# Kernel optimization log

Hardware: AMD Instinct MI355X
Metric: run time of the kernel (lower is better)

The kernel has to match this reference:

```python
import jax, jax.numpy as jnp
import numpy as np

DIM = 256; CTX_DIM = 256; K = 7; SK = 5; NH = 4  # num_heads*2
HD = DIM // NH; SCALE = HD ** -0.5
H = 64; W = 64; HC = 56; WC = 56
LN_EPS = 1e-6; BN_EPS = 1e-5


def make_bias_idx(k, h, w):
    # Faithful port of ContMix.generate_idx + apply_rpb index construction.
    rs = 2 * k - 1
    idx_h = np.arange(k); idx_w = np.arange(k)
    idx_k = (idx_h[:, None] * rs + idx_w).reshape(-1)
    rep_h = np.ones(k, np.int64); rep_h[k // 2] = h - (k - 1)
    rep_w = np.ones(k, np.int64); rep_w[k // 2] = w - (k - 1)
    bias_hw = np.repeat(idx_h, rep_h)[:, None] * rs + np.repeat(idx_w, rep_w)  # (h, w)
    bias_idx = (bias_hw[..., None] + idx_k).reshape(-1, k * k)                 # (h*w, k^2)
    return jnp.asarray(bias_idx[::-1].copy())  # torch.flip along dim 0


def window_idx(n, k):
    # NATTEN-style clamped neighborhood window starts.
    s = np.clip(np.arange(n) - k // 2, 0, n - k)
    return jnp.asarray(s[:, None] + np.arange(k))  # (n, k)


BIDX1 = make_bias_idx(SK, H, W)
BIDX2 = make_bias_idx(K, H, W)
IDXI_S = window_idx(H, SK); IDXJ_S = window_idx(W, SK)
IDXI_L = window_idx(H, K);  IDXJ_L = window_idx(W, K)


def ln2d(x, g, b):
    # LayerNorm over channel dim per spatial location, x: (B, C, H, W)
    mu = x.mean(1, keepdims=True)
    var = ((x - mu) ** 2).mean(1, keepdims=True)
    return (x - mu) * jax.lax.rsqrt(var + LN_EPS) * g[None, :, None, None] + b[None, :, None, None]


def conv1x1(x, Wt):
    return jnp.einsum('oc,bchw->bohw', Wt, x)


def apply_rpb(attn, rpb, bias_idx, h, w):
    g = rpb.shape[0]
    r = rpb.reshape(g, -1)[:, bias_idx]  # (g, h*w, k^2)
    return attn + r.reshape(1, g, h, w, -1)


def na2d_av(attn, value, k, idx_i, idx_j):
    # attn: (B, G, H, W, k^2), value: (B, G, H, W, C)
    B, G, h, w, _ = attn.shape
    v = value[:, :, idx_i]        # (B, G, H, k, W, C)
    v = v[:, :, :, :, idx_j]      # (B, G, H, k, W, k, C)
    a = attn.reshape(B, G, h, w, k, k)
    return jnp.einsum('bghwpq,bghpwqc->bghwc', a, v)


def contmix_forward(x, ctx, Wq, gq, bq, Wk, gk, bk, Wproj, rpb1, rpb2, Wdy, bn_g, bn_b):
    B = x.shape[0]
    q = ln2d(conv1x1(x, Wq), gq, bq) * SCALE                       # (B, DIM, H, W)
    # AdaptiveAvgPool2d(7) on 56x56 -> exact 8x8 bins
    kctx = ctx.reshape(B, CTX_DIM, 7, HC // 7, 7, WC // 7).mean((3, 5))
    kf = ln2d(conv1x1(kctx, Wk), gk, bk)                            # (B, DIM, 7, 7)
    q = q.reshape(B, NH, HD, H * W)
    kf = kf.reshape(B, NH, HD, 49)
    wgt = jnp.einsum('bgcn,bgcl->bgnl', q, kf)                      # (B, 4, HW, 49)
    wgt = jnp.einsum('ml,bgnl->bgnm', Wproj, wgt)                   # (B, 4, HW, 74)
    wgt = wgt.reshape(B, NH, H, W, SK * SK + K * K)
    attn1 = wgt[:, :NH // 2, :, :, :SK * SK]                        # group1, 25
    attn2 = wgt[:, NH // 2:, :, :, SK * SK:]                        # group2, 49
    attn1 = jax.nn.softmax(apply_rpb(attn1, rpb1, BIDX1, H, W), -1)
    attn2 = jax.nn.softmax(apply_rpb(attn2, rpb2, BIDX2, H, W), -1)
    # 'b (m g c) h w -> m b g h w c', m=2, g=2
    v = x.reshape(B, 2, NH // 2, HD, H, W).transpose(1, 0, 2, 4, 5, 3)
    x1 = na2d_av(attn1, v[0], SK, IDXI_S, IDXJ_S)                   # (B, 2, H, W, HD)
    x2 = na2d_av(attn2, v[1], K, IDXI_L, IDXJ_L)
    out = jnp.concatenate([x1, x2], axis=1)                         # (B, 4, H, W, HD)
    out = out.transpose(0, 1, 4, 2, 3).reshape(B, DIM, H, W)
    out = conv1x1(out, Wdy)
    # BatchNorm2d in eval mode: running_mean=0, running_var=1
    out = out * (bn_g * jax.lax.rsqrt(jnp.float32(1.0) + BN_EPS))[None, :, None, None] + bn_b[None, :, None, None]
    return out


def setup_inputs() -> dict:
    key = jax.random.key(0)
    ks = jax.random.split(key, 10)
    d = {}
    d['x'] = jax.random.normal(ks[0], (4, DIM, H, W), jnp.float32)
    d['ctx'] = jax.random.normal(ks[1], (4, CTX_DIM, HC, WC), jnp.float32)
    d['Wq'] = jax.random.normal(ks[2], (DIM, DIM), jnp.float32) * 0.02
    d['gq'] = jnp.ones((DIM,), jnp.float32)
    d['bq'] = jnp.zeros((DIM,), jnp.float32)
    d['Wk'] = jax.random.normal(ks[3], (DIM, CTX_DIM), jnp.float32) * 0.02
    d['gk'] = jnp.ones((DIM,), jnp.float32)
    d['bk'] = jnp.zeros((DIM,), jnp.float32)
    d['Wproj'] = jax.random.normal(ks[4], (SK * SK + K * K, 49), jnp.float32) * 0.1
    d['rpb1'] = jax.random.normal(ks[5], (NH // 2, 2 * SK - 1, 2 * SK - 1), jnp.float32) * 0.02
    d['rpb2'] = jax.random.normal(ks[6], (NH // 2, 2 * K - 1, 2 * K - 1), jnp.float32) * 0.02
    d['Wdy'] = jax.random.normal(ks[7], (DIM, DIM), jnp.float32) * 0.02
    d['bn_g'] = jnp.ones((DIM,), jnp.float32)
    d['bn_b'] = jnp.zeros((DIM,), jnp.float32)
    return d


def reference(x, ctx, Wq, gq, bq, Wk, gk, bk, Wproj, rpb1, rpb2, Wdy, bn_g, bn_b):
    return contmix_forward(x, ctx, Wq, gq, bq, Wk, gk, bk, Wproj, rpb1, rpb2, Wdy, bn_g, bn_b)
```

## Files before the change

### kernel.cpp

```cpp
#include <hip/hip_runtime.h>

#define DEV __device__ __forceinline__

typedef __bf16 bf16x8 __attribute__((ext_vector_type(8)));
typedef __bf16 bf16x4 __attribute__((ext_vector_type(4)));
typedef float floatx4 __attribute__((ext_vector_type(4)));

__global__ __launch_bounds__(256)
void prep_kernel(const float* __restrict__ Wq, const float* __restrict__ Wdy,
                 const float* __restrict__ ctx, const float* __restrict__ x,
                 __bf16* __restrict__ wqb, __bf16* __restrict__ wdyb,
                 float* __restrict__ kctx, __bf16* __restrict__ xt) {
  __shared__ float tile[64][65];
  int bid = blockIdx.x, t = threadIdx.x;
  if (bid < 256) {
    int i = bid * 256 + t;
    wqb[i]  = (__bf16)Wq[i];
    wdyb[i] = (__bf16)Wdy[i];
  } else if (bid < 512) {
    int bc = (bid - 256) * 4 + (t >> 6);
    const float* src = ctx + (size_t)bc * (56 * 56);
    int w = t & 63;
#pragma unroll
    for (int pi = 0; pi < 7; ++pi) {
      float s = 0.f;
      if (w < 56) {
#pragma unroll
        for (int di = 0; di < 8; ++di) s += src[(pi * 8 + di) * 56 + w];
      }
      s += __shfl_down(s, 4);
      s += __shfl_down(s, 2);
      s += __shfl_down(s, 1);
      if (w < 56 && (w & 7) == 0)
        kctx[(size_t)bc * 49 + pi * 7 + (w >> 3)] = s * (1.f / 64.f);
    }
  } else {
    int idx = bid - 512;
    int b = idx >> 8, c0 = ((idx >> 6) & 3) * 64, n0 = (idx & 63) * 64;
    int lane = t & 63, rg = t >> 6;
    const float* src = x + ((size_t)b * 256 + c0) * 4096 + n0;
    for (int i = rg; i < 64; i += 4) tile[i][lane] = src[(size_t)i * 4096 + lane];
    __syncthreads();
    __bf16* dst = xt + ((size_t)b * 4096 + n0) * 256 + c0;
    for (int i = rg; i < 64; i += 4) dst[(size_t)i * 256 + lane] = (__bf16)tile[lane][i];
  }
}

__global__ __launch_bounds__(256)
void kf_ln_kernel(const float* __restrict__ kctx, const float* __restrict__ Wk,
                  const float* __restrict__ gk, const float* __restrict__ bk,
                  float* __restrict__ kf) {
  int b = blockIdx.x / 49, l = blockIdx.x % 49;
  __shared__ float xs[256];
  __shared__ float r1[4], r2[4];
  int o = threadIdx.x;
  xs[o] = kctx[((size_t)b * 256 + o) * 49 + l];
  __syncthreads();
  const float* wrow = Wk + (size_t)o * 256;
  float acc = 0.f;
#pragma unroll 8
  for (int c = 0; c < 256; c += 4) {
    float4 wv = *(const float4*)(wrow + c);
    acc += wv.x * xs[c] + wv.y * xs[c + 1] + wv.z * xs[c + 2] + wv.w * xs[c + 3];
  }
  float s1 = acc, s2 = acc * acc;
#pragma unroll
  for (int off = 32; off > 0; off >>= 1) {
    s1 += __shfl_down(s1, off);
    s2 += __shfl_down(s2, off);
  }
  int wv_ = o >> 6, ln = o & 63;
  if (ln == 0) { r1[wv_] = s1; r2[wv_] = s2; }
  __syncthreads();
  float mu  = (r1[0] + r1[1] + r1[2] + r1[3]) * (1.f / 256.f);
  float var = (r2[0] + r2[1] + r2[2] + r2[3]) * (1.f / 256.f) - mu * mu;
  float rstd = rsqrtf(var + 1e-6f);
  kf[((size_t)b * 256 + o) * 49 + l] = (acc - mu) * rstd * gk[o] + bk[o];
}

__global__ __launch_bounds__(256)
void kfp_kernel(const float* __restrict__ kf, const float* __restrict__ Wproj,
                __bf16* __restrict__ kfpT) {
  int bg = blockIdx.x; int b = bg >> 2, g = bg & 3;
  int m0 = blockIdx.y * 16;
  __shared__ float kfs[64][50];
  __shared__ float wps[16][50];
  int t = threadIdx.x;
  for (int i = t; i < 64 * 49; i += 256) {
    int d = i / 49, l = i % 49;
    kfs[d][l] = kf[((size_t)b * 256 + g * 64 + d) * 49 + l];
  }
  for (int i = t; i < 16 * 49; i += 256) {
    int m = i / 49, l = i % 49;
    wps[m][l] = (m0 + m < 74) ? Wproj[(m0 + m) * 49 + l] : 0.f;
  }
  __syncthreads();
  for (int i = t; i < 64 * 16; i += 256) {
    int d = i >> 4, m = i & 15;
    float s = 0.f;
    if (m0 + m < 74) {
#pragma unroll 7
      for (int l = 0; l < 49; ++l) s += kfs[d][l] * wps[m][l];
    }
    kfpT[(size_t)bg * 5120 + (m0 + m) * 64 + d] = (__bf16)s;
  }
}

DEV int rep_idx(int p, int kc, int t1, int sub) {
  return p < kc ? p : (p < t1 ? kc : p - sub);
}

template <int KK>
DEV void softmax_write(const float* wms, const float* rpb_s, __bf16* __restrict__ attnL,
                       int bg, int n_glob, int row) {
  constexpr int CNT = KK * KK;
  constexpr int RS  = 2 * KK - 1;
  constexpr int KC  = KK / 2;
  constexpr int T1  = KC + (64 - KK + 1);
  constexpr int SUB = 64 - KK;
  constexpr int MLO = (KK == 5) ? 0 : 25;
  constexpr int PW  = (KK == 5) ? 32 : 56;
  int h = n_glob >> 6, w = n_glob & 63;
  int rh = rep_idx(63 - h, KC, T1, SUB);
  int rw = rep_idx(63 - w, KC, T1, SUB);
  float vals[CNT];
  float mx = -1e30f;
#pragma unroll
  for (int m = 0; m < CNT; ++m) {
    int ki = m / KK, kj = m % KK;
    float v = wms[row * 81 + MLO + m] + rpb_s[(rh + ki) * RS + rw + kj];
    vals[m] = v; mx = fmaxf(mx, v);
  }
  float ssum = 0.f;
#pragma unroll
  for (int m = 0; m < CNT; ++m) { float e = __expf(vals[m] - mx); vals[m] = e; ssum += e; }
  float inv = 1.f / ssum;
  __bf16 hv[PW];
#pragma unroll
  for (int m = 0; m < PW; ++m) hv[m] = (__bf16)(m < CNT ? vals[m] * inv : 0.f);
  __bf16* ap = attnL + ((size_t)bg * 4096 + n_glob) * 56;
#pragma unroll
  for (int i = 0; i < PW / 8; ++i) *(bf16x8*)(ap + i * 8) = *(bf16x8*)&hv[i * 8];
}

__global__ __launch_bounds__(256, 2)
void qattn_kernel(const __bf16* __restrict__ Wb, const __bf16* __restrict__ XT,
                  const __bf16* __restrict__ kfpT,
                  const float* __restrict__ gq, const float* __restrict__ bq,
                  const float* __restrict__ rpb1, const float* __restrict__ rpb2,
                  __bf16* __restrict__ attnL) {
  __shared__ float wms[128 * 81];
  __shared__ float rpb_s[500];
  __shared__ float gqs[256], bqs[256];
  __shared__ float red_s[128], red_q[128];
  __shared__ float st_mu[32], st_rs[32];
  __bf16* As  = (__bf16*)wms;
  __bf16* Bs  = (__bf16*)wms + 8192;
  __bf16* Aat = (__bf16*)wms;

  int b  = blockIdx.z;
  int n0 = blockIdx.x * 32;
  int t  = threadIdx.x;
  int lane = t & 63, wv = t >> 6;
  int col = lane & 15, quad = lane >> 4;

  gqs[t] = gq[t] * 0.125f;
  bqs[t] = bq[t] * 0.125f;
  for (int i = t; i < 162; i += 256) rpb_s[i] = rpb1[i];
  for (int i = t; i < 338; i += 256) rpb_s[162 + i] = rpb2[i];

  floatx4 acc[4][2];
#pragma unroll
  for (int i = 0; i < 4; ++i)
#pragma unroll
    for (int j = 0; j < 2; ++j) acc[i][j] = {0.f, 0.f, 0.f, 0.f};

  const __bf16* wp = Wb + (size_t)t * 256;
  int rowB = t >> 3, kB = (t & 7) * 4;
  const __bf16* xp = XT + ((size_t)b * 4096 + n0 + rowB) * 256 + kB;
  bf16x8 ra0 = *(const bf16x8*)(wp + 0);
  bf16x8 ra1 = *(const bf16x8*)(wp + 8);
  bf16x8 ra2 = *(const bf16x8*)(wp + 16);
  bf16x8 ra3 = *(const bf16x8*)(wp + 24);
  bf16x4 rb  = *(const bf16x4*)xp;

  for (int c0 = 0; c0 < 256; c0 += 32) {
    *(bf16x8*)&As[t * 32 + 0]  = ra0;
    *(bf16x8*)&As[t * 32 + 8]  = ra1;
    *(bf16x8*)&As[t * 32 + 16] = ra2;
    *(bf16x8*)&As[t * 32 + 24] = ra3;
    *(bf16x4*)&Bs[rowB * 32 + kB] = rb;
    __syncthreads();
    if (c0 + 32 < 256) {
      ra0 = *(const bf16x8*)(wp + c0 + 32);
      ra1 = *(const bf16x8*)(wp + c0 + 40);
      ra2 = *(const bf16x8*)(wp + c0 + 48);
      ra3 = *(const bf16x8*)(wp + c0 + 56);
      rb  = *(const bf16x4*)(xp + c0 + 32);
    }
    bf16x8 fa[4], fb[2];
#pragma unroll
    for (int i = 0; i < 4; ++i)
      fa[i] = *(const bf16x8*)&As[(wv * 64 + i * 16 + col) * 32 + quad * 8];
#pragma unroll
    for (int j = 0; j < 2; ++j)
      fb[j] = *(const bf16x8*)&Bs[(j * 16 + col) * 32 + quad * 8];
#pragma unroll
    for (int i = 0; i < 4; ++i)
#pragma unroll
      for (int j = 0; j < 2; ++j)
        acc[i][j] = __builtin_amdgcn_mfma_f32_16x16x32_bf16(fa[i], fb[j], acc[i][j], 0, 0, 0);
    __syncthreads();
  }

#pragma unroll
  for (int j = 0; j < 2; ++j) {
    float s = 0.f, q = 0.f;
#pragma unroll
    for (int i = 0; i < 4; ++i)
#pragma unroll
      for (int r = 0; r < 4; ++r) { float v = acc[i][j][r]; s += v; q += v * v; }
    s += __shfl_xor(s, 16); s += __shfl_xor(s, 32);
    q += __shfl_xor(q, 16); q += __shfl_xor(q, 32);
    if (quad == 0) {
      red_s[wv * 32 + j * 16 + col] = s;
      red_q[wv * 32 + j * 16 + col] = q;
    }
  }
  __syncthreads();
  if (t < 32) {
    float s = red_s[t] + red_s[32 + t] + red_s[64 + t] + red_s[96 + t];
    float q = red_q[t] + red_q[32 + t] + red_q[64 + t] + red_q[96 + t];
    float mu  = s * (1.f / 256.f);
    float var = q * (1.f / 256.f) - mu * mu;
    st_mu[t] = mu;
    st_rs[t] = rsqrtf(var + 1e-6f);
  }
  __syncthreads();

#pragma unroll
  for (int j = 0; j < 2; ++j) {
    float mu = st_mu[j * 16 + col], rs = st_rs[j * 16 + col];
#pragma unroll
    for (int i = 0; i < 4; ++i) {
      __bf16 pk[4];
#pragma unroll
      for (int r = 0; r < 4; ++r) {
        int o = wv * 64 + i * 16 + quad * 4 + r;
        pk[r] = (__bf16)((acc[i][j][r] - mu) * rs * gqs[o] + bqs[o]);
      }
      *(bf16x4*)&Aat[(wv * 32 + j * 16 + col) * 72 + i * 16 + quad * 4] = *(bf16x4*)pk;
    }
  }
  __syncthreads();

  bf16x8 fa2[2][2], fb2[2][5];
  const __bf16* kp = kfpT + (size_t)(b * 4 + wv) * 5120;
#pragma unroll
  for (int ks = 0; ks < 2; ++ks) {
#pragma unroll
    for (int a = 0; a < 2; ++a)
      fa2[ks][a] = *(const bf16x8*)&Aat[(wv * 32 + a * 16 + col) * 72 + ks * 32 + quad * 8];
#pragma unroll
    for (int nt = 0; nt < 5; ++nt)
      fb2[ks][nt] = *(const bf16x8*)&kp[(nt * 16 + col) * 64 + ks * 32 + quad * 8];
  }
  floatx4 acc2[2][5];
#pragma unroll
  for (int a = 0; a < 2; ++a)
#pragma unroll
    for (int nt = 0; nt < 5; ++nt) acc2[a][nt] = {0.f, 0.f, 0.f, 0.f};
#pragma unroll
  for (int ks = 0; ks < 2; ++ks)
#pragma unroll
    for (int a = 0; a < 2; ++a)
#pragma unroll
      for (int nt = 0; nt < 5; ++nt)
        acc2[a][nt] = __builtin_amdgcn_mfma_f32_16x16x32_bf16(fa2[ks][a], fb2[ks][nt], acc2[a][nt], 0, 0, 0);
  __syncthreads();

#pragma unroll
  for (int a = 0; a < 2; ++a)
#pragma unroll
    for (int nt = 0; nt < 5; ++nt)
#pragma unroll
      for (int r = 0; r < 4; ++r)
        wms[(wv * 32 + a * 16 + quad * 4 + r) * 81 + nt * 16 + col] = acc2[a][nt][r];
  __syncthreads();

  if (t < 128) {
    int g2 = t >> 5;
    int n_glob = n0 + (t & 31);
    int bg = b * 4 + g2;
    if (g2 < 2) softmax_write<5>(wms, rpb_s + g2 * 81,              attnL, bg, n_glob, t);
    else        softmax_write<7>(wms, rpb_s + 162 + (g2 - 2) * 169, attnL, bg, n_glob, t);
  }
}

template <int MODE>
__global__ __launch_bounds__(256, 2)
void conv_mfma_kernel(const __bf16* __restrict__ Wb, const __bf16* __restrict__ Xin,
                      void* __restrict__ Yout, float* __restrict__ stats,
                      const float* __restrict__ bn_g, const float* __restrict__ bn_b) {
  int b  = blockIdx.z;
  int n0 = blockIdx.x * 128;
  int o0 = blockIdx.y * 128;
  __shared__ __bf16 As[128 * 32];
  __shared__ __bf16 Bs[128 * 32];
  int t = threadIdx.x;
  int lane = t & 63, wv = t >> 6;
  int mq = (wv & 1) * 64, nq = (wv >> 1) * 64;
  int col = lane & 15, quad = lane >> 4;
  floatx4 acc[4][4];
#pragma unroll
  for (int i = 0; i < 4; ++i)
#pragma unroll
    for (int j = 0; j < 4; ++j) acc[i][j] = {0.f, 0.f, 0.f, 0.f};
  int sm = t >> 1, sk = (t & 1) << 4;
  const __bf16* wp = Wb + (size_t)(o0 + sm) * 256 + sk;
  auto xaddr = [&](int c0) -> const __bf16* {
    if (MODE == 0) {
      return Xin + ((size_t)b * 4096 + n0 + sm) * 256 + c0 + sk;
    } else {
      int c = c0 + sk, g = c >> 6, c64 = c & 63;
      return Xin + (((size_t)(b * 4 + g)) * 4096 + n0 + sm) * 64 + c64;
    }
  };
  bf16x8 wa0 = *(const bf16x8*)wp;
  bf16x8 wa1 = *(const bf16x8*)(wp + 8);
  const __bf16* x0 = xaddr(0);
  bf16x8 xb0 = *(const bf16x8*)x0;
  bf16x8 xb1 = *(const bf16x8*)(x0 + 8);
  for (int c0 = 0; c0 < 256; c0 += 32) {
    *(bf16x8*)&As[sm * 32 + sk]     = wa0;
    *(bf16x8*)&As[sm * 32 + sk + 8] = wa1;
    *(bf16x8*)&Bs[sm * 32 + sk]     = xb0;
    *(bf16x8*)&Bs[sm * 32 + sk + 8] = xb1;
    __syncthreads();
    if (c0 + 32 < 256) {
      wa0 = *(const bf16x8*)(wp + c0 + 32);
      wa1 = *(const bf16x8*)(wp + c0 + 40);
      const __bf16* xn = xaddr(c0 + 32);
      xb0 = *(const bf16x8*)xn;
      xb1 = *(const bf16x8*)(xn + 8);
    }
    bf16x8 fa[4], fb[4];
#pragma unroll
    for (int i = 0; i < 4; ++i)
      fa[i] = *(const bf16x8*)&As[(mq + i * 16 + col) * 32 + quad * 8];
#pragma unroll
    for (int j = 0; j < 4; ++j)
      fb[j] = *(const bf16x8*)&Bs[(nq + j * 16 + col) * 32 + quad * 8];
#pragma unroll
    for (int i = 0; i < 4; ++i)
#pragma unroll
      for (int j = 0; j < 4; ++j)
        acc[i][j] = __builtin_amdgcn_mfma_f32_16x16x32_bf16(fa[i], fb[j], acc[i][j], 0, 0, 0);
    __syncthreads();
  }
  {
    float* Yf = (float*)Yout + (size_t)b * 256 * 4096;
#pragma unroll
    for (int i = 0; i < 4; ++i) {
#pragma unroll
      for (int r = 0; r < 4; ++r) {
        int o = o0 + mq + i * 16 + quad * 4 + r;
        float scale = bn_g[o] * 0.9999950000374997f;
        float shift = bn_b[o];
        float* yrow = Yf + (size_t)o * 4096 + n0 + nq + col;
#pragma unroll
        for (int j = 0; j < 4; ++j) yrow[j * 16] = acc[i][j][r] * scale + shift;
      }
    }
  }
}

template <int KK>
DEV void na2d_body(const __bf16* __restrict__ attnL, const __bf16* __restrict__ XT,
                   __bf16* __restrict__ midT, __bf16* xs, int bg, int h0, int chalf, int t) {
  constexpr int CNT = KK * KK, KC = KK / 2, SMAX = 64 - KK;
  constexpr int ROWS = KK + 3;
  constexpr int PW = (KK == 5) ? 32 : 56;
  int b = bg >> 2, g = bg & 3;
  int si0 = min(max(h0 - KC, 0), SMAX);
  {
    int sn = t >> 2, sc = t & 3;
    const __bf16* src = XT + ((size_t)b * 4096 + sn) * 256 + g * 64 + chalf * 32 + sc * 8;
#pragma unroll
    for (int r = 0; r < ROWS; ++r) {
      int gr = min(si0 + r, 63);
      *(bf16x8*)&xs[(r * 64 + sn) * 40 + sc * 8] = *(const bf16x8*)(src + (size_t)gr * 64 * 256);
    }
  }
  __syncthreads();
  int w = t >> 2, cg = t & 3;
  int sj = min(max(w - KC, 0), SMAX);
#pragma unroll
  for (int h4 = 0; h4 < 4; ++h4) {
    int h = h0 + h4;
    int base = min(max(h - KC, 0), SMAX) - si0;
    bf16x8 avh[PW / 8];
    const __bf16* ap = attnL + ((size_t)bg * 4096 + h * 64 + w) * 56;
#pragma unroll
    for (int i = 0; i < PW / 8; ++i) avh[i] = *(const bf16x8*)(ap + i * 8);
    float av[CNT];
#pragma unroll
    for (int m = 0; m < CNT; ++m) av[m] = (float)avh[m / 8][m % 8];
    float acc[8] = {};
#pragma unroll
    for (int p = 0; p < KK; ++p) {
      const __bf16* xr = &xs[((base + p) * 64 + sj) * 40 + cg * 8];
#pragma unroll
      for (int q = 0; q < KK; ++q) {
        bf16x8 v = *(const bf16x8*)(xr + q * 40);
        float a = av[p * KK + q];
#pragma unroll
        for (int e = 0; e < 8; ++e) acc[e] += a * (float)v[e];
      }
    }
    __bf16 hv[8];
#pragma unroll
    for (int e = 0; e < 8; ++e) hv[e] = (__bf16)acc[e];
    *(bf16x8*)&midT[((size_t)bg * 4096 + h * 64 + w) * 64 + chalf * 32 + cg * 8] = *(bf16x8*)hv;
  }
}

__global__ __launch_bounds__(256)
void na2d_kernel(const __bf16* __restrict__ attnL, const __bf16* __restrict__ XT,
                 __bf16* __restrict__ midT) {
  __shared__ __bf16 xs[10 * 64 * 40];
  int bg = blockIdx.x, h0 = blockIdx.y * 4, chalf = blockIdx.z, t = threadIdx.x;
  if ((bg & 3) < 2) na2d_body<5>(attnL, XT, midT, xs, bg, h0, chalf, t);
  else              na2d_body<7>(attnL, XT, midT, xs, bg, h0, chalf, t);
}

extern "C" void kernel_launch(void* const* d_in, const int* in_sizes, int n_in,
                              void* d_out, int out_size, void* d_ws, size_t ws_size,
                              hipStream_t stream) {
  const float* x     = (const float*)d_in[0];
  const float* ctx   = (const float*)d_in[1];
  const float* Wq    = (const float*)d_in[2];
  const float* gq    = (const float*)d_in[3];
  const float* bq    = (const float*)d_in[4];
  const float* Wk    = (const float*)d_in[5];
  const float* gk    = (const float*)d_in[6];
  const float* bk    = (const float*)d_in[7];
  const float* Wproj = (const float*)d_in[8];
  const float* rpb1  = (const float*)d_in[9];
  const float* rpb2  = (const float*)d_in[10];
  const float* Wdy   = (const float*)d_in[11];
  const float* bn_g  = (const float*)d_in[12];
  const float* bn_b  = (const float*)d_in[13];
  float* out = (float*)d_out;

  float* ws     = (float*)d_ws;
  float* kctx   = ws;
  float* kf     = kctx + 50176;
  __bf16* attnL = (__bf16*)(kf + 50176);
  __bf16* wqb   = attnL + 3670016;
  __bf16* wdyb  = wqb + 65536;
  __bf16* kfpT  = wdyb + 65536;
  __bf16* XT    = kfpT + 81920;
  __bf16* midT  = XT + 4194304;

  prep_kernel<<<dim3(1536), dim3(256), 0, stream>>>(Wq, Wdy, ctx, x, wqb, wdyb, kctx, XT);
  kf_ln_kernel<<<dim3(196), dim3(256), 0, stream>>>(kctx, Wk, gk, bk, kf);
  kfp_kernel<<<dim3(16, 5), dim3(256), 0, stream>>>(kf, Wproj, kfpT);
  qattn_kernel<<<dim3(128, 1, 4), dim3(256), 0, stream>>>(wqb, XT, kfpT, gq, bq, rpb1, rpb2, attnL);
  na2d_kernel<<<dim3(16, 16, 2), dim3(256), 0, stream>>>(attnL, XT, midT);
  conv_mfma_kernel<1><<<dim3(32, 2, 4), dim3(256), 0, stream>>>(wdyb, midT, out, nullptr, bn_g, bn_b);
}
```

Baseline: 163.9 us.

## Double qattn tile to 64 pixels with 512-thread blocks sharing the weight tile

The qattn kernel now covers 64 pixels per block with 8 waves instead of 32 pixels with 4 waves. Each weight tile is loaded once and reused across two pixel halves, which halves total Wq traffic and the grid size. The cost is a larger shared-memory footprint (about 83KB for wms), so one block per CU. Only 256 blocks remain, which may leave CUs idle or reduce latency hiding.

New measurement: 160.5 us. 1.02x faster.

```diff
diff --git a/kernel.cpp b/kernel.cpp
--- a/kernel.cpp
+++ b/kernel.cpp
@@ -143,31 +143,34 @@
   for (int i = 0; i < PW / 8; ++i) *(bf16x8*)(ap + i * 8) = *(bf16x8*)&hv[i * 8];
 }
 
-__global__ __launch_bounds__(256, 2)
+__global__ __launch_bounds__(512, 1)
 void qattn_kernel(const __bf16* __restrict__ Wb, const __bf16* __restrict__ XT,
                   const __bf16* __restrict__ kfpT,
                   const float* __restrict__ gq, const float* __restrict__ bq,
                   const float* __restrict__ rpb1, const float* __restrict__ rpb2,
                   __bf16* __restrict__ attnL) {
-  __shared__ float wms[128 * 81];
+  __shared__ float wms[256 * 81];
   __shared__ float rpb_s[500];
   __shared__ float gqs[256], bqs[256];
-  __shared__ float red_s[128], red_q[128];
-  __shared__ float st_mu[32], st_rs[32];
+  __shared__ float red_s[4][64], red_q[4][64];
+  __shared__ float st_mu[64], st_rs[64];
   __bf16* As  = (__bf16*)wms;
   __bf16* Bs  = (__bf16*)wms + 8192;
   __bf16* Aat = (__bf16*)wms;
 
   int b  = blockIdx.z;
-  int n0 = blockIdx.x * 32;
+  int n0 = blockIdx.x * 64;
   int t  = threadIdx.x;
   int lane = t & 63, wv = t >> 6;
+  int oq = wv & 3, nh = wv >> 2;
   int col = lane & 15, quad = lane >> 4;
 
-  gqs[t] = gq[t] * 0.125f;
-  bqs[t] = bq[t] * 0.125f;
-  for (int i = t; i < 162; i += 256) rpb_s[i] = rpb1[i];
-  for (int i = t; i < 338; i += 256) rpb_s[162 + i] = rpb2[i];
+  if (t < 256) {
+    gqs[t] = gq[t] * 0.125f;
+    bqs[t] = bq[t] * 0.125f;
+  }
+  for (int i = t; i < 162; i += 512) rpb_s[i] = rpb1[i];
+  for (int i = t; i < 338; i += 512) rpb_s[162 + i] = rpb2[i];
 
   floatx4 acc[4][2];
 #pragma unroll
@@ -175,36 +178,31 @@
 #pragma unroll
     for (int j = 0; j < 2; ++j) acc[i][j] = {0.f, 0.f, 0.f, 0.f};
 
-  const __bf16* wp = Wb + (size_t)t * 256;
+  int rowA = t >> 1, halfA = (t & 1) * 16;
   int rowB = t >> 3, kB = (t & 7) * 4;
+  const __bf16* wp = Wb + (size_t)rowA * 256 + halfA;
   const __bf16* xp = XT + ((size_t)b * 4096 + n0 + rowB) * 256 + kB;
-  bf16x8 ra0 = *(const bf16x8*)(wp + 0);
+  bf16x8 ra0 = *(const bf16x8*)wp;
   bf16x8 ra1 = *(const bf16x8*)(wp + 8);
-  bf16x8 ra2 = *(const bf16x8*)(wp + 16);
-  bf16x8 ra3 = *(const bf16x8*)(wp + 24);
   bf16x4 rb  = *(const bf16x4*)xp;
 
   for (int c0 = 0; c0 < 256; c0 += 32) {
-    *(bf16x8*)&As[t * 32 + 0]  = ra0;
-    *(bf16x8*)&As[t * 32 + 8]  = ra1;
-    *(bf16x8*)&As[t * 32 + 16] = ra2;
-    *(bf16x8*)&As[t * 32 + 24] = ra3;
-    *(bf16x4*)&Bs[rowB * 32 + kB] = rb;
+    *(bf16x8*)&As[rowA * 32 + halfA]     = ra0;
+    *(bf16x8*)&As[rowA * 32 + halfA + 8] = ra1;
+    *(bf16x4*)&Bs[rowB * 32 + kB]        = rb;
     __syncthreads();
     if (c0 + 32 < 256) {
       ra0 = *(const bf16x8*)(wp + c0 + 32);
       ra1 = *(const bf16x8*)(wp + c0 + 40);
-      ra2 = *(const bf16x8*)(wp + c0 + 48);
-      ra3 = *(const bf16x8*)(wp + c0 + 56);
       rb  = *(const bf16x4*)(xp + c0 + 32);
     }
     bf16x8 fa[4], fb[2];
 #pragma unroll
     for (int i = 0; i < 4; ++i)
-      fa[i] = *(const bf16x8*)&As[(wv * 64 + i * 16 + col) * 32 + quad * 8];
+      fa[i] = *(const bf16x8*)&As[(oq * 64 + i * 16 + col) * 32 + quad * 8];
 #pragma unroll
     for (int j = 0; j < 2; ++j)
-      fb[j] = *(const bf16x8*)&Bs[(j * 16 + col) * 32 + quad * 8];
+      fb[j] = *(const bf16x8*)&Bs[(nh * 32 + j * 16 + col) * 32 + quad * 8];
 #pragma unroll
     for (int i = 0; i < 4; ++i)
 #pragma unroll
@@ -223,14 +221,14 @@
     s += __shfl_xor(s, 16); s += __shfl_xor(s, 32);
     q += __shfl_xor(q, 16); q += __shfl_xor(q, 32);
     if (quad == 0) {
-      red_s[wv * 32 + j * 16 + col] = s;
-      red_q[wv * 32 + j * 16 + col] = q;
-    }
-  }
-  __syncthreads();
-  if (t < 32) {
-    float s = red_s[t] + red_s[32 + t] + red_s[64 + t] + red_s[96 + t];
-    float q = red_q[t] + red_q[32 + t] + red_q[64 + t] + red_q[96 + t];
+      red_s[oq][nh * 32 + j * 16 + col] = s;
+      red_q[oq][nh * 32 + j * 16 + col] = q;
+    }
+  }
+  __syncthreads();
+  if (t < 64) {
+    float s = red_s[0][t] + red_s[1][t] + red_s[2][t] + red_s[3][t];
+    float q = red_q[0][t] + red_q[1][t] + red_q[2][t] + red_q[3][t];
     float mu  = s * (1.f / 256.f);
     float var = q * (1.f / 256.f) - mu * mu;
     st_mu[t] = mu;
@@ -240,27 +238,28 @@
 
 #pragma unroll
   for (int j = 0; j < 2; ++j) {
-    float mu = st_mu[j * 16 + col], rs = st_rs[j * 16 + col];
+    int n_loc = nh * 32 + j * 16 + col;
+    float mu = st_mu[n_loc], rs = st_rs[n_loc];
 #pragma unroll
     for (int i = 0; i < 4; ++i) {
       __bf16 pk[4];
 #pragma unroll
       for (int r = 0; r < 4; ++r) {
-        int o = wv * 64 + i * 16 + quad * 4 + r;
+        int o = oq * 64 + i * 16 + quad * 4 + r;
         pk[r] = (__bf16)((acc[i][j][r] - mu) * rs * gqs[o] + bqs[o]);
       }
-      *(bf16x4*)&Aat[(wv * 32 + j * 16 + col) * 72 + i * 16 + quad * 4] = *(bf16x4*)pk;
+      *(bf16x4*)&Aat[((size_t)(oq * 64 + n_loc)) * 72 + i * 16 + quad * 4] = *(bf16x4*)pk;
     }
   }
   __syncthreads();
 
   bf16x8 fa2[2][2], fb2[2][5];
-  const __bf16* kp = kfpT + (size_t)(b * 4 + wv) * 5120;
+  const __bf16* kp = kfpT + (size_t)(b * 4 + oq) * 5120;
 #pragma unroll
   for (int ks = 0; ks < 2; ++ks) {
 #pragma unroll
     for (int a = 0; a < 2; ++a)
-      fa2[ks][a] = *(const bf16x8*)&Aat[(wv * 32 + a * 16 + col) * 72 + ks * 32 + quad * 8];
+      fa2[ks][a] = *(const bf16x8*)&Aat[((size_t)(oq * 64 + nh * 32 + a * 16 + col)) * 72 + ks * 32 + quad * 8];
 #pragma unroll
     for (int nt = 0; nt < 5; ++nt)
       fb2[ks][nt] = *(const bf16x8*)&kp[(nt * 16 + col) * 64 + ks * 32 + quad * 8];
@@ -285,12 +284,12 @@
     for (int nt = 0; nt < 5; ++nt)
 #pragma unroll
       for (int r = 0; r < 4; ++r)
-        wms[(wv * 32 + a * 16 + quad * 4 + r) * 81 + nt * 16 + col] = acc2[a][nt][r];
-  __syncthreads();
-
-  if (t < 128) {
-    int g2 = t >> 5;
-    int n_glob = n0 + (t & 31);
+        wms[(oq * 64 + nh * 32 + a * 16 + quad * 4 + r) * 81 + nt * 16 + col] = acc2[a][nt][r];
+  __syncthreads();
+
+  if (t < 256) {
+    int g2 = t >> 6;
+    int n_glob = n0 + (t & 63);
     int bg = b * 4 + g2;
     if (g2 < 2) softmax_write<5>(wms, rpb_s + g2 * 81,              attnL, bg, n_glob, t);
     else        softmax_write<7>(wms, rpb_s + 162 + (g2 - 2) * 169, attnL, bg, n_glob, t);
@@ -466,7 +465,7 @@
   prep_kernel<<<dim3(1536), dim3(256), 0, stream>>>(Wq, Wdy, ctx, x, wqb, wdyb, kctx, XT);
   kf_ln_kernel<<<dim3(196), dim3(256), 0, stream>>>(kctx, Wk, gk, bk, kf);
   kfp_kernel<<<dim3(16, 5), dim3(256), 0, stream>>>(kf, Wproj, kfpT);
-  qattn_kernel<<<dim3(128, 1, 4), dim3(256), 0, stream>>>(wqb, XT, kfpT, gq, bq, rpb1, rpb2, attnL);
+  qattn_kernel<<<dim3(64, 1, 4), dim3(512), 0, stream>>>(wqb, XT, kfpT, gq, bq, rpb1, rpb2, attnL);
   na2d_kernel<<<dim3(16, 16, 2), dim3(256), 0, stream>>>(attnL, XT, midT);
   conv_mfma_kernel<1><<<dim3(32, 2, 4), dim3(256), 0, stream>>>(wdyb, midT, out, nullptr, bn_g, bn_b);
 }
```
